# Kernel tuning notes

Measured on AMD Instinct MI355X. Metric: run time of the kernel, lower is better.

The kernel has to match this reference:

```python
import jax, jax.numpy as jnp
import numpy as np

B, S, D, H = 4, 2048, 1024, 16
HD = D // H
SCALE = HD ** -0.5


def setup_inputs() -> dict:
    key = jax.random.key(0)
    ks = jax.random.split(key, 5)
    std = D ** -0.5
    return {
        "x": jax.random.normal(ks[0], (B, S, D), jnp.float32),
        "wq": jax.random.normal(ks[1], (D, D), jnp.float32) * std,
        "bq": jnp.zeros((D,), jnp.float32),
        "wk": jax.random.normal(ks[2], (D, D), jnp.float32) * std,
        "bk": jnp.zeros((D,), jnp.float32),
        "wv": jax.random.normal(ks[3], (D, D), jnp.float32) * std,
        "bv": jnp.zeros((D,), jnp.float32),
        "wo": jax.random.normal(ks[4], (D, D), jnp.float32) * std,
        "bo": jnp.zeros((D,), jnp.float32),
    }


def reference(x, wq, bq, wk, bk, wv, bv, wo, bo):
    # projections; weights stored as [in, out] so y = x @ w + b
    q = (x @ wq + bq).reshape(B, S, H, HD).transpose(0, 2, 1, 3)  # [B,H,S,HD]
    k = (x @ wk + bk).reshape(B, S, H, HD).transpose(0, 2, 1, 3)
    v = (x @ wv + bv).reshape(B, S, H, HD).transpose(0, 2, 1, 3)
    attn = jnp.einsum("bhqd,bhkd->bhqk", q, k) * SCALE  # [B,H,S,S]
    attn = jax.nn.softmax(attn, axis=-1)
    out = jnp.einsum("bhqk,bhkd->bhqd", attn, v)  # [B,H,S,HD]
    out = out.transpose(0, 2, 1, 3).reshape(B, S, D)
    return out @ wo + bo
```

## Files before the change

### kernel.cpp

```cpp
#include <hip/hip_runtime.h>
#include <stdint.h>


typedef __attribute__((ext_vector_type(8))) short bf16x8;
typedef __attribute__((ext_vector_type(4))) short bf16x4;
typedef __attribute__((ext_vector_type(4))) float f32x4;
typedef unsigned short u16;
typedef unsigned int u32;

#define AS1 __attribute__((address_space(1)))
#define AS3 __attribute__((address_space(3)))

#define SCALE_L2E 0.18033688011112042f

__device__ __forceinline__ void gld_lds16(const void* g, void* l) {
  __builtin_amdgcn_global_load_lds((const AS1 void*)g, (AS3 void*)l, 16, 0, 0);
}

__device__ __forceinline__ u16 f2bf(float f) {
  u32 x = __builtin_bit_cast(u32, f);
  x += 0x7fff + ((x >> 16) & 1);
  return (u16)(x >> 16);
}

__device__ __forceinline__ u16 f2bf_fast(float a) {
#if __has_builtin(__builtin_amdgcn_cvt_pk_bf16_f32)
  auto v = __builtin_amdgcn_cvt_pk_bf16_f32(a, a);
  return (u16)(__builtin_bit_cast(u32, v) & 0xffffu);
#else
  return f2bf(a);
#endif
}

__device__ __forceinline__ bf16x4 pack_bf16x4(float a, float b, float c, float d) {
#if __has_builtin(__builtin_amdgcn_cvt_pk_bf16_f32)
  u32 lo = __builtin_bit_cast(u32, __builtin_amdgcn_cvt_pk_bf16_f32(a, b));
  u32 hi = __builtin_bit_cast(u32, __builtin_amdgcn_cvt_pk_bf16_f32(c, d));
#else
  u32 lo = (u32)f2bf(a) | ((u32)f2bf(b) << 16);
  u32 hi = (u32)f2bf(c) | ((u32)f2bf(d) << 16);
#endif
  union { u32 w[2]; bf16x4 v; } u;
  u.w[0] = lo; u.w[1] = hi;
  return u.v;
}

__device__ __forceinline__ f32x4 mfma16(bf16x4 a, bf16x4 b, f32x4 c) {
#if __has_builtin(__builtin_amdgcn_mfma_f32_16x16x16_bf16)
  return __builtin_amdgcn_mfma_f32_16x16x16_bf16(a, b, c, 0, 0, 0);
#else
  return __builtin_amdgcn_mfma_f32_16x16x16bf16_1k(a, b, c, 0, 0, 0);
#endif
}

__device__ __forceinline__ float exp2_fast(float x) {
#if __has_builtin(__builtin_amdgcn_exp2f)
  return __builtin_amdgcn_exp2f(x);
#else
  return exp2f(x);
#endif
}

__global__ __launch_bounds__(256) void convert_x(const float* __restrict__ x,
                                                 u16* __restrict__ xb) {
  int i = (blockIdx.x * 256 + threadIdx.x) * 4;
  float4 v = *(const float4*)(x + i);
  ushort4 o;
  o.x = f2bf(v.x); o.y = f2bf(v.y); o.z = f2bf(v.z); o.w = f2bf(v.w);
  *(ushort4*)(xb + i) = o;
}

__global__ __launch_bounds__(256) void pack_weights(
    const float* __restrict__ wq, const float* __restrict__ wk,
    const float* __restrict__ wv, const float* __restrict__ wo,
    u16* __restrict__ wt_qkv, u16* __restrict__ wt_o) {
  __shared__ float tile[64][65];
  int mat = blockIdx.z;
  const float* src = (mat == 0) ? wq : (mat == 1) ? wk : (mat == 2) ? wv : wo;
  int k0 = blockIdx.y * 64, j0 = blockIdx.x * 64;
  int t = threadIdx.x;
  int lr = t >> 6;
  int lc = t & 63;
#pragma unroll
  for (int it = 0; it < 16; ++it) {
    int r = it * 4 + lr;
    tile[r][lc] = src[(size_t)(k0 + r) * 1024 + j0 + lc];
  }
  __syncthreads();
  u16* dst = (mat == 3) ? wt_o : (wt_qkv + (size_t)mat * 1024 * 1024);
#pragma unroll
  for (int it = 0; it < 16; ++it) {
    int nl = it * 4 + lr;
    float v = tile[lc][nl];
    if (mat == 0) v *= SCALE_L2E;
    dst[(size_t)(j0 + nl) * 1024 + k0 + lc] = f2bf(v);
  }
}

template <int MODE>
__global__ __launch_bounds__(256, 2) void gemm_bt(
    const u16* __restrict__ A, const u16* __restrict__ Bt,
    const float* __restrict__ bias0, const float* __restrict__ bias1,
    const float* __restrict__ bias2,
    void* __restrict__ out0v, void* __restrict__ out1v, void* __restrict__ out2v) {
  __shared__ u16 lA[128 * 32];
  __shared__ u16 lB[128 * 32];
  const int K = 1024;
  int tid = threadIdx.x;
  int wave = tid >> 6, lane = tid & 63;

  int bid = blockIdx.x;
  int m0, n0;
  if constexpr (MODE == 0) {
    int xcd = bid & 7, j = bid >> 3;
    n0 = (xcd * 3 + j % 3) * 128;
    m0 = (j / 3) * 128;
  } else {
    n0 = (bid & 7) * 128;
    m0 = (bid >> 3) * 128;
  }
  int wm = (wave & 1) * 64, wn = (wave >> 1) * 64;

  f32x4 acc[4][4];
#pragma unroll
  for (int i = 0; i < 4; ++i)
#pragma unroll
    for (int j = 0; j < 4; ++j) acc[i][j] = f32x4{0.f, 0.f, 0.f, 0.f};

  int srow = lane >> 2;
  int scol = (lane & 3) * 8;

  for (int k0 = 0; k0 < K; k0 += 32) {
#pragma unroll
    for (int c = 0; c < 2; ++c) {
      int rbase = wave * 32 + c * 16;
      gld_lds16(A + (size_t)(m0 + rbase + srow) * K + k0 + scol, lA + rbase * 32);
      gld_lds16(Bt + (size_t)(n0 + rbase + srow) * K + k0 + scol, lB + rbase * 32);
    }
    __syncthreads();
    bf16x8 af[4], bfr[4];
#pragma unroll
    for (int mt = 0; mt < 4; ++mt)
      af[mt] = *(const bf16x8*)(lA + (wm + mt * 16 + (lane & 15)) * 32 + (lane >> 4) * 8);
#pragma unroll
    for (int nt = 0; nt < 4; ++nt)
      bfr[nt] = *(const bf16x8*)(lB + (wn + nt * 16 + (lane & 15)) * 32 + (lane >> 4) * 8);
#pragma unroll
    for (int mt = 0; mt < 4; ++mt)
#pragma unroll
      for (int nt = 0; nt < 4; ++nt)
        acc[mt][nt] = __builtin_amdgcn_mfma_f32_16x16x32_bf16(af[mt], bfr[nt], acc[mt][nt], 0, 0, 0);
    __syncthreads();
  }

  int rbase0 = m0 + wm + (lane >> 4) * 4;
  int cbase = n0 + wn + (lane & 15);
#pragma unroll
  for (int nt = 0; nt < 4; ++nt) {
    int col = cbase + nt * 16;
    if constexpr (MODE == 0) {
      int mat = col >> 10, j = col & 1023;
      const float* bp = (mat == 0) ? bias0 : (mat == 1) ? bias1 : bias2;
      float bv = bp[j];
      if (mat == 0) bv *= SCALE_L2E;
      int h = j >> 6, hd = j & 63;
      if (mat == 2) {
        u16* base = (u16*)out2v;
#pragma unroll
        for (int mt = 0; mt < 4; ++mt) {
          int row0 = rbase0 + mt * 16;
          int b = row0 >> 11, s = row0 & 2047;
          int ci = s >> 6, sg = (s >> 2) & 15;
          int slot = (hd + 4 * sg) & 63;
          size_t off = (size_t)(b * 16 + h) * 131072 + ci * 4096 + sg * 256 + slot * 4;
          ushort4 pk;
          pk.x = f2bf_fast(acc[mt][nt][0] + bv);
          pk.y = f2bf_fast(acc[mt][nt][1] + bv);
          pk.z = f2bf_fast(acc[mt][nt][2] + bv);
          pk.w = f2bf_fast(acc[mt][nt][3] + bv);
          *(ushort4*)(base + off) = pk;
        }
      } else {
        u16* base = (mat == 0) ? (u16*)out0v : (u16*)out1v;
#pragma unroll
        for (int mt = 0; mt < 4; ++mt)
#pragma unroll
          for (int r = 0; r < 4; ++r) {
            int row = rbase0 + mt * 16 + r;
            int b = row >> 11, s = row & 2047;
            size_t idx = ((size_t)(b * 16 + h) * 2048 + s) * 64 + hd;
            base[idx] = f2bf_fast(acc[mt][nt][r] + bv);
          }
      }
    } else {
      float bv = bias0[col];
      float* o = (float*)out0v;
#pragma unroll
      for (int mt = 0; mt < 4; ++mt)
#pragma unroll
        for (int r = 0; r < 4; ++r) {
          int row = rbase0 + mt * 16 + r;
          o[(size_t)row * 1024 + col] = acc[mt][nt][r] + bv;
        }
    }
  }
}

__global__ __launch_bounds__(256, 2) void flash_attn(
    const u16* __restrict__ Q, const u16* __restrict__ Kb,
    const u16* __restrict__ Vg, u16* __restrict__ ctx) {
  __shared__ u16 lK[2][64 * 32];
  __shared__ u16 lV[4096];
  int tid = threadIdx.x, wave = tid >> 6, lane = tid & 63;

  int F = blockIdx.x;
  int xcd = F & 7, idx = F >> 3;
  int bh = xcd * 8 + (idx >> 3);
  int q0 = (idx & 7) * 256;
  int b = bh >> 4, h = bh & 15;
  const u16* Qp = Q + (size_t)bh * 2048 * 64;
  const u16* Kp = Kb + (size_t)bh * 2048 * 64;
  const u16* Vp = Vg + (size_t)bh * 131072;

  int c = lane & 15, g = lane >> 4;

  bf16x8 qf[4][2];
#pragma unroll
  for (int t = 0; t < 4; ++t) {
    const u16* qrow = Qp + (size_t)(q0 + wave * 64 + t * 16 + c) * 64 + g * 8;
    qf[t][0] = *(const bf16x8*)qrow;
    qf[t][1] = *(const bf16x8*)(qrow + 32);
  }

  float lsum[4] = {0.f, 0.f, 0.f, 0.f};
  f32x4 o[4][4];
#pragma unroll
  for (int t = 0; t < 4; ++t)
#pragma unroll
    for (int dt = 0; dt < 4; ++dt) o[t][dt] = f32x4{0.f, 0.f, 0.f, 0.f};

  int srow = lane >> 2;
  int schunk = (((lane & 3) ^ ((lane >> 3) & 3)) * 8);
  int rsw = (c >> 1) & 3;
  int stg_row = wave * 16 + srow;
  int vrot = c + 4 * g;

  for (int s0 = 0; s0 < 2048; s0 += 64) {
#pragma unroll
    for (int kk = 0; kk < 2; ++kk)
      gld_lds16(Kp + (size_t)(s0 + stg_row) * 64 + kk * 32 + schunk,
                lK[kk] + wave * 512);
#pragma unroll
    for (int vv = 0; vv < 2; ++vv)
      gld_lds16(Vp + (size_t)s0 * 64 + wave * 1024 + vv * 512 + lane * 8,
                lV + wave * 1024 + vv * 512);
    __syncthreads();

#pragma unroll
    for (int st = 0; st < 4; ++st) {
      bf16x8 kf0 = *(const bf16x8*)(lK[0] + (st * 16 + c) * 32 + (g ^ rsw) * 8);
      bf16x8 kf1 = *(const bf16x8*)(lK[1] + (st * 16 + c) * 32 + (g ^ rsw) * 8);

      bf16x4 pf[4];
#pragma unroll
      for (int t = 0; t < 4; ++t) {
        f32x4 sa = __builtin_amdgcn_mfma_f32_16x16x32_bf16(kf0, qf[t][0],
                       f32x4{0.f, 0.f, 0.f, 0.f}, 0, 0, 0);
        sa = __builtin_amdgcn_mfma_f32_16x16x32_bf16(kf1, qf[t][1], sa, 0, 0, 0);
        float p0 = exp2_fast(sa[0]), p1 = exp2_fast(sa[1]);
        float p2 = exp2_fast(sa[2]), p3 = exp2_fast(sa[3]);
        lsum[t] += (p0 + p1) + (p2 + p3);
        pf[t] = pack_bf16x4(p0, p1, p2, p3);
      }

      int sg = st * 4 + g;
      int rotb = (vrot + 16 * st) & 63;
#pragma unroll
      for (int dt = 0; dt < 4; ++dt) {
        bf16x4 vf = *(const bf16x4*)(lV + sg * 256 + (((rotb + dt * 16) & 63) << 2));
#pragma unroll
        for (int t = 0; t < 4; ++t)
          o[t][dt] = mfma16(vf, pf[t], o[t][dt]);
      }
    }
    __syncthreads();
  }

#pragma unroll
  for (int t = 0; t < 4; ++t) {
    float rs = lsum[t];
    rs += __shfl_xor(rs, 16);
    rs += __shfl_xor(rs, 32);
    float inv = 1.0f / fmaxf(rs, 1e-30f);
    int q = q0 + wave * 64 + t * 16 + c;
    size_t rowbase = ((size_t)(b * 2048 + q) * 16 + h) * 64;
#pragma unroll
    for (int dt = 0; dt < 4; ++dt) {
      ushort4 pk;
      pk.x = f2bf_fast(o[t][dt][0] * inv);
      pk.y = f2bf_fast(o[t][dt][1] * inv);
      pk.z = f2bf_fast(o[t][dt][2] * inv);
      pk.w = f2bf_fast(o[t][dt][3] * inv);
      *(ushort4*)(ctx + rowbase + dt * 16 + g * 4) = pk;
    }
  }
}

extern "C" void kernel_launch(void* const* d_in, const int* in_sizes, int n_in,
                              void* d_out, int out_size, void* d_ws, size_t ws_size,
                              hipStream_t stream) {
  const float* x  = (const float*)d_in[0];
  const float* wq = (const float*)d_in[1];
  const float* bq = (const float*)d_in[2];
  const float* wk = (const float*)d_in[3];
  const float* bk = (const float*)d_in[4];
  const float* wv = (const float*)d_in[5];
  const float* bv = (const float*)d_in[6];
  const float* wo = (const float*)d_in[7];
  const float* bo = (const float*)d_in[8];

  u16* ws = (u16*)d_ws;
  u16* xb     = ws;
  u16* wt_qkv = xb + (size_t)8192 * 1024;
  u16* wt_o   = wt_qkv + (size_t)3072 * 1024;
  u16* Qb     = wt_o + (size_t)1024 * 1024;
  u16* Kbuf   = Qb + (size_t)8192 * 1024;
  u16* Vgb    = Kbuf + (size_t)8192 * 1024;
  u16* ctx    = Vgb + (size_t)8192 * 1024;

  convert_x<<<8192, 256, 0, stream>>>(x, xb);
  pack_weights<<<dim3(16, 16, 4), 256, 0, stream>>>(wq, wk, wv, wo, wt_qkv, wt_o);
  gemm_bt<0><<<1536, 256, 0, stream>>>(xb, wt_qkv, bq, bk, bv, Qb, Kbuf, Vgb);
  flash_attn<<<512, 256, 0, stream>>>(Qb, Kbuf, Vgb, ctx);
  gemm_bt<1><<<512, 256, 0, stream>>>(ctx, wt_o, bo, nullptr, nullptr,
                                      d_out, nullptr, nullptr);
}
```

Before: 289.2 us.

## Use 16x16x32 MFMA for PV via LDS-staged P and transposed V layout

V is now written transposed ([bh][hd][s]) by the QKV GEMM epilogue and loaded into LDS with the same swizzle as K. The P tile is written to a per-wave LDS scratch so the PV product can use the wider 16x16x32 bf16 MFMA instead of 16x16x16. This halves the PV MFMA instruction count but adds LDS write/read traffic for P and extra shared memory, which could affect occupancy.

Result: slower. 299.7 us (+3.6%).

```diff
diff --git a/kernel.cpp b/kernel.cpp
--- a/kernel.cpp
+++ b/kernel.cpp
@@ -3,8 +3,8 @@
 
 
 typedef __attribute__((ext_vector_type(8))) short bf16x8;
-typedef __attribute__((ext_vector_type(4))) short bf16x4;
 typedef __attribute__((ext_vector_type(4))) float f32x4;
+typedef __attribute__((ext_vector_type(2))) unsigned int u32x2;
 typedef unsigned short u16;
 typedef unsigned int u32;
 
@@ -32,24 +32,11 @@
 #endif
 }
 
-__device__ __forceinline__ bf16x4 pack_bf16x4(float a, float b, float c, float d) {
+__device__ __forceinline__ u32 pk2(float a, float b) {
 #if __has_builtin(__builtin_amdgcn_cvt_pk_bf16_f32)
-  u32 lo = __builtin_bit_cast(u32, __builtin_amdgcn_cvt_pk_bf16_f32(a, b));
-  u32 hi = __builtin_bit_cast(u32, __builtin_amdgcn_cvt_pk_bf16_f32(c, d));
+  return __builtin_bit_cast(u32, __builtin_amdgcn_cvt_pk_bf16_f32(a, b));
 #else
-  u32 lo = (u32)f2bf(a) | ((u32)f2bf(b) << 16);
-  u32 hi = (u32)f2bf(c) | ((u32)f2bf(d) << 16);
-#endif
-  union { u32 w[2]; bf16x4 v; } u;
-  u.w[0] = lo; u.w[1] = hi;
-  return u.v;
-}
-
-__device__ __forceinline__ f32x4 mfma16(bf16x4 a, bf16x4 b, f32x4 c) {
-#if __has_builtin(__builtin_amdgcn_mfma_f32_16x16x16_bf16)
-  return __builtin_amdgcn_mfma_f32_16x16x16_bf16(a, b, c, 0, 0, 0);
-#else
-  return __builtin_amdgcn_mfma_f32_16x16x16bf16_1k(a, b, c, 0, 0, 0);
+  return (u32)f2bf(a) | ((u32)f2bf(b) << 16);
 #endif
 }
 
@@ -170,15 +157,13 @@
         for (int mt = 0; mt < 4; ++mt) {
           int row0 = rbase0 + mt * 16;
           int b = row0 >> 11, s = row0 & 2047;
-          int ci = s >> 6, sg = (s >> 2) & 15;
-          int slot = (hd + 4 * sg) & 63;
-          size_t off = (size_t)(b * 16 + h) * 131072 + ci * 4096 + sg * 256 + slot * 4;
+          size_t idx = ((size_t)(b * 16 + h) * 64 + hd) * 2048 + s;
           ushort4 pk;
           pk.x = f2bf_fast(acc[mt][nt][0] + bv);
           pk.y = f2bf_fast(acc[mt][nt][1] + bv);
           pk.z = f2bf_fast(acc[mt][nt][2] + bv);
           pk.w = f2bf_fast(acc[mt][nt][3] + bv);
-          *(ushort4*)(base + off) = pk;
+          *(ushort4*)(base + idx) = pk;
         }
       } else {
         u16* base = (mat == 0) ? (u16*)out0v : (u16*)out1v;
@@ -208,9 +193,10 @@
 
 __global__ __launch_bounds__(256, 2) void flash_attn(
     const u16* __restrict__ Q, const u16* __restrict__ Kb,
-    const u16* __restrict__ Vg, u16* __restrict__ ctx) {
+    const u16* __restrict__ Vt, u16* __restrict__ ctx) {
   __shared__ u16 lK[2][64 * 32];
-  __shared__ u16 lV[4096];
+  __shared__ u16 lV[2][64 * 32];
+  __shared__ u32 lP[4][64 * 20];
   int tid = threadIdx.x, wave = tid >> 6, lane = tid & 63;
 
   int F = blockIdx.x;
@@ -220,7 +206,7 @@
   int b = bh >> 4, h = bh & 15;
   const u16* Qp = Q + (size_t)bh * 2048 * 64;
   const u16* Kp = Kb + (size_t)bh * 2048 * 64;
-  const u16* Vp = Vg + (size_t)bh * 131072;
+  const u16* Vp = Vt + (size_t)bh * 64 * 2048;
 
   int c = lane & 15, g = lane >> 4;
 
@@ -243,44 +229,48 @@
   int schunk = (((lane & 3) ^ ((lane >> 3) & 3)) * 8);
   int rsw = (c >> 1) & 3;
   int stg_row = wave * 16 + srow;
-  int vrot = c + 4 * g;
+  u32* pb = lP[wave];
 
   for (int s0 = 0; s0 < 2048; s0 += 64) {
 #pragma unroll
-    for (int kk = 0; kk < 2; ++kk)
+    for (int kk = 0; kk < 2; ++kk) {
       gld_lds16(Kp + (size_t)(s0 + stg_row) * 64 + kk * 32 + schunk,
                 lK[kk] + wave * 512);
-#pragma unroll
-    for (int vv = 0; vv < 2; ++vv)
-      gld_lds16(Vp + (size_t)s0 * 64 + wave * 1024 + vv * 512 + lane * 8,
-                lV + wave * 1024 + vv * 512);
+      gld_lds16(Vp + (size_t)stg_row * 2048 + s0 + kk * 32 + schunk,
+                lV[kk] + wave * 512);
+    }
     __syncthreads();
 
 #pragma unroll
-    for (int st = 0; st < 4; ++st) {
-      bf16x8 kf0 = *(const bf16x8*)(lK[0] + (st * 16 + c) * 32 + (g ^ rsw) * 8);
-      bf16x8 kf1 = *(const bf16x8*)(lK[1] + (st * 16 + c) * 32 + (g ^ rsw) * 8);
-
-      bf16x4 pf[4];
+    for (int kk = 0; kk < 2; ++kk) {
+#pragma unroll
+      for (int stl = 0; stl < 2; ++stl) {
+        int st = kk * 2 + stl;
+        bf16x8 kf0 = *(const bf16x8*)(lK[0] + (st * 16 + c) * 32 + (g ^ rsw) * 8);
+        bf16x8 kf1 = *(const bf16x8*)(lK[1] + (st * 16 + c) * 32 + (g ^ rsw) * 8);
+#pragma unroll
+        for (int t = 0; t < 4; ++t) {
+          f32x4 sa = __builtin_amdgcn_mfma_f32_16x16x32_bf16(kf0, qf[t][0],
+                         f32x4{0.f, 0.f, 0.f, 0.f}, 0, 0, 0);
+          sa = __builtin_amdgcn_mfma_f32_16x16x32_bf16(kf1, qf[t][1], sa, 0, 0, 0);
+          float p0 = exp2_fast(sa[0]), p1 = exp2_fast(sa[1]);
+          float p2 = exp2_fast(sa[2]), p3 = exp2_fast(sa[3]);
+          lsum[t] += (p0 + p1) + (p2 + p3);
+          u32x2 w; w.x = pk2(p0, p1); w.y = pk2(p2, p3);
+          *(u32x2*)(pb + (t * 16 + c) * 20 + stl * 8 + 2 * g) = w;
+        }
+      }
+
+      bf16x8 vf[4];
+#pragma unroll
+      for (int dt = 0; dt < 4; ++dt)
+        vf[dt] = *(const bf16x8*)(lV[kk] + (dt * 16 + c) * 32 + (g ^ rsw) * 8);
 #pragma unroll
       for (int t = 0; t < 4; ++t) {
-        f32x4 sa = __builtin_amdgcn_mfma_f32_16x16x32_bf16(kf0, qf[t][0],
-                       f32x4{0.f, 0.f, 0.f, 0.f}, 0, 0, 0);
-        sa = __builtin_amdgcn_mfma_f32_16x16x32_bf16(kf1, qf[t][1], sa, 0, 0, 0);
-        float p0 = exp2_fast(sa[0]), p1 = exp2_fast(sa[1]);
-        float p2 = exp2_fast(sa[2]), p3 = exp2_fast(sa[3]);
-        lsum[t] += (p0 + p1) + (p2 + p3);
-        pf[t] = pack_bf16x4(p0, p1, p2, p3);
-      }
-
-      int sg = st * 4 + g;
-      int rotb = (vrot + 16 * st) & 63;
-#pragma unroll
-      for (int dt = 0; dt < 4; ++dt) {
-        bf16x4 vf = *(const bf16x4*)(lV + sg * 256 + (((rotb + dt * 16) & 63) << 2));
-#pragma unroll
-        for (int t = 0; t < 4; ++t)
-          o[t][dt] = mfma16(vf, pf[t], o[t][dt]);
+        bf16x8 pfr = *(const bf16x8*)(pb + (t * 16 + c) * 20 + 4 * g);
+#pragma unroll
+        for (int dt = 0; dt < 4; ++dt)
+          o[t][dt] = __builtin_amdgcn_mfma_f32_16x16x32_bf16(vf[dt], pfr, o[t][dt], 0, 0, 0);
       }
     }
     __syncthreads();
@@ -325,13 +315,13 @@
   u16* wt_o   = wt_qkv + (size_t)3072 * 1024;
   u16* Qb     = wt_o + (size_t)1024 * 1024;
   u16* Kbuf   = Qb + (size_t)8192 * 1024;
-  u16* Vgb    = Kbuf + (size_t)8192 * 1024;
-  u16* ctx    = Vgb + (size_t)8192 * 1024;
+  u16* Vtb    = Kbuf + (size_t)8192 * 1024;
+  u16* ctx    = Vtb + (size_t)8192 * 1024;
 
   convert_x<<<8192, 256, 0, stream>>>(x, xb);
   pack_weights<<<dim3(16, 16, 4), 256, 0, stream>>>(wq, wk, wv, wo, wt_qkv, wt_o);
-  gemm_bt<0><<<1536, 256, 0, stream>>>(xb, wt_qkv, bq, bk, bv, Qb, Kbuf, Vgb);
-  flash_attn<<<512, 256, 0, stream>>>(Qb, Kbuf, Vgb, ctx);
+  gemm_bt<0><<<1536, 256, 0, stream>>>(xb, wt_qkv, bq, bk, bv, Qb, Kbuf, Vtb);
+  flash_attn<<<512, 256, 0, stream>>>(Qb, Kbuf, Vtb, ctx);
   gemm_bt<1><<<512, 256, 0, stream>>>(ctx, wt_o, bo, nullptr, nullptr,
                                       d_out, nullptr, nullptr);
 }
```
